# Kernel optimization log

Hardware: AMD Instinct MI355X
Metric: run time of the kernel (lower is better)

Reference implementation:

```python
import jax, jax.numpy as jnp
import numpy as np

INPUT_SIZE = 256
OUTPUT_SIZE = 128
N = 8192
SLOPE = 0.01
NEG_BIG = -9e15


def setup_inputs() -> dict:
    key = jax.random.key(0)
    k_h, k_adj, k_W, k_a = jax.random.split(key, 4)
    h = jax.random.normal(k_h, (N, INPUT_SIZE), dtype=jnp.float32)
    adj = jax.random.randint(k_adj, (N, N), 0, 2, dtype=jnp.int32)
    # xavier_uniform with gain=1.414
    gain = 1.414
    lim_W = gain * np.sqrt(6.0 / (INPUT_SIZE + OUTPUT_SIZE))
    W = jax.random.uniform(k_W, (INPUT_SIZE, OUTPUT_SIZE), dtype=jnp.float32, minval=-lim_W, maxval=lim_W)
    lim_a = gain * np.sqrt(6.0 / (2 * OUTPUT_SIZE + 1))
    a = jax.random.uniform(k_a, (2 * OUTPUT_SIZE, 1), dtype=jnp.float32, minval=-lim_a, maxval=lim_a)
    return {"h": h, "adj": adj, "W": W, "a": a}


def reference(h, adj, W, a):
    # Wh: [N, F]
    Wh = h @ W
    Fo = Wh.shape[1]
    # Original builds [N, N, 2F] concat then matmul with a; equivalent to
    # e[i, j] = leaky_relu(Wh[i] . a[:F] + Wh[j] . a[F:]) via broadcasting.
    src = Wh @ a[:Fo, 0]   # [N]
    dst = Wh @ a[Fo:, 0]   # [N]
    e = jax.nn.leaky_relu(src[:, None] + dst[None, :], negative_slope=SLOPE)  # [N, N]
    att = jnp.where(adj > 0, e, NEG_BIG)
    att = jax.nn.softmax(att, axis=1)
    return att @ Wh
```

## Files before the change

### kernel.cpp

```cpp
#include <hip/hip_runtime.h>
#include <hip/hip_bf16.h>

typedef unsigned short u16;
typedef unsigned int u32;
typedef __attribute__((ext_vector_type(8))) short short8;
typedef __attribute__((ext_vector_type(4))) float f32x4;

#define NN 8192
#define KIN 256
#define FOUT 128
#define SPLITS 8
#define KPER (NN / SPLITS)
#define BK 64
#define ITERS (KPER / BK)
#define L2E 1.4426950408889634f

__device__ __forceinline__ float exp2fast(float x) { return __builtin_amdgcn_exp2f(x); }

__device__ __forceinline__ u16 f2bf(float f) {
    u32 u = __float_as_uint(f);
    u32 r = ((u >> 16) & 1u) + 0x7fffu;
    return (u16)((u + r) >> 16);
}
__device__ __forceinline__ u32 fkey(float f) {
    u32 b = __float_as_uint(f);
    return (b & 0x80000000u) ? ~b : (b | 0x80000000u);
}
__device__ __forceinline__ float funkey(u32 k) {
    u32 b = (k & 0x80000000u) ? (k & 0x7fffffffu) : ~k;
    return __uint_as_float(b);
}

__global__ __launch_bounds__(256) void k1_wh(
    const float* __restrict__ h, const float* __restrict__ W, const float* __restrict__ a,
    u16* __restrict__ whbt,
    float* __restrict__ src, float* __restrict__ dst, u32* __restrict__ gmaxk)
{
    __shared__ float hT[64][36];
    __shared__ u16   lt[128][40];
    __shared__ float sd[32][2];
    const int t  = threadIdx.x;
    const int m0 = blockIdx.x * 32;
    const int rq = t >> 5, cq = t & 31;

    float acc[4][4];
#pragma unroll
    for (int i = 0; i < 4; i++)
#pragma unroll
        for (int j = 0; j < 4; j++) acc[i][j] = 0.f;
    if (t < 64) sd[t >> 1][t & 1] = 0.f;

    for (int kt = 0; kt < KIN; kt += 64) {
        __syncthreads();
#pragma unroll
        for (int s2 = 0; s2 < 2; s2++) {
            int f = s2 * 256 + t;
            int r = f >> 4, kc = (f & 15) * 4;
            float4 hv = *(const float4*)(h + (size_t)(m0 + r) * KIN + kt + kc);
            hT[kc + 0][r] = hv.x; hT[kc + 1][r] = hv.y;
            hT[kc + 2][r] = hv.z; hT[kc + 3][r] = hv.w;
        }
        __syncthreads();
        for (int k = 0; k < 64; k++) {
            float4 wv = *(const float4*)(W + (size_t)(kt + k) * FOUT + cq * 4);
            float h0 = hT[k][rq * 4 + 0], h1 = hT[k][rq * 4 + 1];
            float h2 = hT[k][rq * 4 + 2], h3 = hT[k][rq * 4 + 3];
            acc[0][0] += h0 * wv.x; acc[0][1] += h0 * wv.y; acc[0][2] += h0 * wv.z; acc[0][3] += h0 * wv.w;
            acc[1][0] += h1 * wv.x; acc[1][1] += h1 * wv.y; acc[1][2] += h1 * wv.z; acc[1][3] += h1 * wv.w;
            acc[2][0] += h2 * wv.x; acc[2][1] += h2 * wv.y; acc[2][2] += h2 * wv.z; acc[2][3] += h2 * wv.w;
            acc[3][0] += h3 * wv.x; acc[3][1] += h3 * wv.y; acc[3][2] += h3 * wv.z; acc[3][3] += h3 * wv.w;
        }
    }
#pragma unroll
    for (int i = 0; i < 4; i++) {
        float sp = 0.f, dp = 0.f;
#pragma unroll
        for (int j = 0; j < 4; j++) {
            sp += acc[i][j] * a[cq * 4 + j];
            dp += acc[i][j] * a[FOUT + cq * 4 + j];
            lt[cq * 4 + j][rq * 4 + i] = f2bf(acc[i][j]);
        }
        atomicAdd(&sd[rq * 4 + i][0], sp);
        atomicAdd(&sd[rq * 4 + i][1], dp);
    }
    __syncthreads();
    if (t < 32) { src[m0 + t] = sd[t][0]; dst[m0 + t] = sd[t][1]; }
    if (t < 64) {
        float v = (t < 32) ? sd[t][1] : -3.0e38f;
#pragma unroll
        for (int off = 32; off >= 1; off >>= 1) v = fmaxf(v, __shfl_down(v, off));
        if (t == 0) atomicMax(gmaxk, fkey(v));
    }
#pragma unroll
    for (int s2 = 0; s2 < 2; s2++) {
        int f = s2 * 256 + t;
        int n = f >> 2;
        int q = (f & 3) * 8;
        uint4 v = *(const uint4*)&lt[n][q];
        *(uint4*)(whbt + (size_t)n * NN + m0 + q) = v;
    }
}

__global__ __launch_bounds__(256, 2) void k2_attn(
    const int* __restrict__ adj, const float* __restrict__ src, const float* __restrict__ dst,
    const u16* __restrict__ whbt, const u32* __restrict__ gmaxk,
    float* __restrict__ accp, float* __restrict__ lp)
{
    __shared__ u16 P[128][72];
    __shared__ u16 Bs[128][72];
    __shared__ float2 sC[128];
    __shared__ float lred[128][16];
    const int t = threadIdx.x;
    const int i0 = blockIdx.x * 128;
    const int split = blockIdx.y;
    const int kb0 = split * KPER;
    const int lane = t & 63, wave = t >> 6;
    const int mw = (wave >> 1) * 64, nw = (wave & 1) * 64;
    const int l15 = lane & 15, quad = lane >> 4;
    const int g = t >> 4, c4 = (t & 15) * 4;

    if (t < 128) {
        float s = src[i0 + t] * L2E;
        float gm = funkey(*gmaxk) * L2E;
        float x = s + gm;
        sC[t] = make_float2(s, fmaxf(x, 0.01f * x));
    }
    float psum[8];
#pragma unroll
    for (int s2 = 0; s2 < 8; s2++) psum[s2] = 0.f;
    f32x4 acc[4][4];
#pragma unroll
    for (int mt = 0; mt < 4; mt++)
#pragma unroll
        for (int nt = 0; nt < 4; nt++) acc[mt][nt] = {0.f, 0.f, 0.f, 0.f};

    int4 av[8]; float4 dv; uint4 bv[4];
    {
        float4 d = *(const float4*)(dst + kb0 + c4);
        dv = make_float4(d.x * L2E, d.y * L2E, d.z * L2E, d.w * L2E);
    }
#pragma unroll
    for (int s2 = 0; s2 < 8; s2++)
        av[s2] = *(const int4*)(adj + (size_t)(i0 + 16 * s2 + g) * NN + kb0 + c4);
#pragma unroll
    for (int p = 0; p < 4; p++) {
        int f = p * 256 + t;
        int n = f >> 3, seg = (f & 7) * 8;
        bv[p] = *(const uint4*)(whbt + (size_t)n * NN + kb0 + seg);
    }

    for (int it = 0; it < ITERS; ++it) {
        const int kb = kb0 + it * BK;
        __syncthreads();
        float4 d4 = dv;
#pragma unroll
        for (int s2 = 0; s2 < 8; s2++) {
            int r = 16 * s2 + g;
            float2 sc = sC[r];
            int4 a4 = av[s2];
            float x0 = sc.x + d4.x; x0 = fmaxf(x0, 0.01f * x0);
            float x1 = sc.x + d4.y; x1 = fmaxf(x1, 0.01f * x1);
            float x2 = sc.x + d4.z; x2 = fmaxf(x2, 0.01f * x2);
            float x3 = sc.x + d4.w; x3 = fmaxf(x3, 0.01f * x3);
            float p0 = (a4.x > 0) ? exp2fast(x0 - sc.y) : 0.f;
            float p1 = (a4.y > 0) ? exp2fast(x1 - sc.y) : 0.f;
            float p2 = (a4.z > 0) ? exp2fast(x2 - sc.y) : 0.f;
            float p3 = (a4.w > 0) ? exp2fast(x3 - sc.y) : 0.f;
            psum[s2] += (p0 + p1) + (p2 + p3);
            u32 lo = (u32)f2bf(p0) | ((u32)f2bf(p1) << 16);
            u32 hi = (u32)f2bf(p2) | ((u32)f2bf(p3) << 16);
            *(uint2*)&P[r][c4] = make_uint2(lo, hi);
        }
#pragma unroll
        for (int p = 0; p < 4; p++) {
            int f = p * 256 + t;
            int n = f >> 3, seg = (f & 7) * 8;
            *(uint4*)&Bs[n][seg] = bv[p];
        }
        __syncthreads();
        if (it + 1 < ITERS) {
            int kbn = kb + BK;
            float4 d = *(const float4*)(dst + kbn + c4);
            dv = make_float4(d.x * L2E, d.y * L2E, d.z * L2E, d.w * L2E);
#pragma unroll
            for (int s2 = 0; s2 < 8; s2++)
                av[s2] = *(const int4*)(adj + (size_t)(i0 + 16 * s2 + g) * NN + kbn + c4);
#pragma unroll
            for (int p = 0; p < 4; p++) {
                int f = p * 256 + t;
                int n = f >> 3, seg = (f & 7) * 8;
                bv[p] = *(const uint4*)(whbt + (size_t)n * NN + kbn + seg);
            }
        }
#pragma unroll
        for (int ks = 0; ks < 2; ks++) {
            int kk = ks * 32 + quad * 8;
            short8 af[4], bfr[4];
#pragma unroll
            for (int mt = 0; mt < 4; mt++)
                af[mt] = *(const short8*)&P[mw + mt * 16 + l15][kk];
#pragma unroll
            for (int nt = 0; nt < 4; nt++)
                bfr[nt] = *(const short8*)&Bs[nw + nt * 16 + l15][kk];
#pragma unroll
            for (int mt = 0; mt < 4; mt++)
#pragma unroll
                for (int nt = 0; nt < 4; nt++)
                    acc[mt][nt] = __builtin_amdgcn_mfma_f32_16x16x32_bf16(
                        af[mt], bfr[nt], acc[mt][nt], 0, 0, 0);
        }
    }
    __syncthreads();
#pragma unroll
    for (int s2 = 0; s2 < 8; s2++) lred[16 * s2 + g][t & 15] = psum[s2];
    __syncthreads();
    if (t < 128) {
        float s = 0.f;
#pragma unroll
        for (int j = 0; j < 16; j++) s += lred[t][j];
        lp[split * NN + i0 + t] = s;
    }
    float* ab = accp + (size_t)split * (NN * FOUT);
#pragma unroll
    for (int mt = 0; mt < 4; mt++)
#pragma unroll
        for (int nt = 0; nt < 4; nt++) {
            int row = i0 + mw + mt * 16 + quad * 4;
            int col = nw + nt * 16 + l15;
#pragma unroll
            for (int reg = 0; reg < 4; reg++)
                ab[(size_t)(row + reg) * FOUT + col] = acc[mt][nt][reg];
        }
}

__global__ __launch_bounds__(256) void k3_comb(
    const float* __restrict__ accp, const float* __restrict__ lp, float* __restrict__ out)
{
    int idx = blockIdx.x * 256 + threadIdx.x;
    int i = idx >> 5;
    float4 s = make_float4(0.f, 0.f, 0.f, 0.f);
    float l = 0.f;
#pragma unroll
    for (int sp = 0; sp < SPLITS; sp++) {
        float4 v = *(const float4*)(accp + (size_t)sp * (NN * FOUT) + (size_t)idx * 4);
        s.x += v.x; s.y += v.y; s.z += v.z; s.w += v.w;
        l += lp[sp * NN + i];
    }
    float inv = 1.0f / l;
    *(float4*)(out + (size_t)idx * 4) = make_float4(s.x * inv, s.y * inv, s.z * inv, s.w * inv);
}

extern "C" void kernel_launch(void* const* d_in, const int* in_sizes, int n_in,
                              void* d_out, int out_size, void* d_ws, size_t ws_size,
                              hipStream_t stream) {
    const float* h   = (const float*)d_in[0];
    const int*   adj = (const int*)d_in[1];
    const float* W   = (const float*)d_in[2];
    const float* a   = (const float*)d_in[3];
    float* out = (float*)d_out;

    char* ws = (char*)d_ws;
    u16*   whbt  = (u16*)ws;
    float* src   = (float*)(ws + (2u << 20));
    float* dst   = src + NN;
    u32*   gmaxk = (u32*)(dst + NN);
    float* accp  = (float*)(ws + (3u << 20));
    float* lp    = (float*)(ws + (35u << 20));

    (void)hipMemsetAsync(gmaxk, 0, sizeof(u32), stream);
    k1_wh<<<dim3(NN / 32), dim3(256), 0, stream>>>(h, W, a, whbt, src, dst, gmaxk);
    k2_attn<<<dim3(NN / 128, SPLITS), dim3(256), 0, stream>>>(adj, src, dst, whbt, gmaxk, accp, lp);
    k3_comb<<<dim3((NN * FOUT / 4) / 256), dim3(256), 0, stream>>>(accp, lp, out);
}
```

Baseline: 482.4 us.

## Shrink attention tile to 64 rows, raise occupancy, stagger k-iterations across blocks

Halves the k2 row tile from 128 to 64 and raises the launch bound from 2 to 4 blocks per SIMD, so each wave now computes a 64x32 output slab. Adjacent blocks start their K loop at staggered offsets to spread accesses across memory channels. The leaky-relu is folded algebraically into a max of two precomputed affine terms, masking is done by clamping the exponent, and bf16 conversion uses a packed intrinsic. Partial results are stored in MFMA-native tile layout and row sums are reduced with shuffles, which adds a small row-sum kernel and a scattered-write combine step. The smaller tile doubles the Wh B-tile traffic per output row.

```diff
diff --git a/kernel.cpp b/kernel.cpp
--- a/kernel.cpp
+++ b/kernel.cpp
@@ -22,6 +22,11 @@
     u32 r = ((u >> 16) & 1u) + 0x7fffu;
     return (u16)((u + r) >> 16);
 }
+__device__ __forceinline__ u32 pk_bf16(float a, float b) {
+    union { __hip_bfloat162 h2; u32 u; } cv;
+    cv.h2 = __float22bfloat162_rn(make_float2(a, b));
+    return cv.u;
+}
 __device__ __forceinline__ u32 fkey(float f) {
     u32 b = __float_as_uint(f);
     return (b & 0x80000000u) ? ~b : (b | 0x80000000u);
@@ -101,75 +106,76 @@
     }
 }
 
-__global__ __launch_bounds__(256, 2) void k2_attn(
+__global__ __launch_bounds__(256, 4) void k2_attn(
     const int* __restrict__ adj, const float* __restrict__ src, const float* __restrict__ dst,
     const u16* __restrict__ whbt, const u32* __restrict__ gmaxk,
     float* __restrict__ accp, float* __restrict__ lp)
 {
-    __shared__ u16 P[128][72];
+    __shared__ u16 P[64][72];
     __shared__ u16 Bs[128][72];
-    __shared__ float2 sC[128];
-    __shared__ float lred[128][16];
+    __shared__ float2 sY[64];
     const int t = threadIdx.x;
-    const int i0 = blockIdx.x * 128;
+    const int bx = blockIdx.x;
+    const int i0 = bx * 64;
     const int split = blockIdx.y;
     const int kb0 = split * KPER;
     const int lane = t & 63, wave = t >> 6;
-    const int mw = (wave >> 1) * 64, nw = (wave & 1) * 64;
+    const int nw = wave * 32;
     const int l15 = lane & 15, quad = lane >> 4;
-    const int g = t >> 4, c4 = (t & 15) * 4;
-
-    if (t < 128) {
+    const int g = t >> 4;
+    const int c4 = (t & 15) * 4;
+
+    if (t < 64) {
         float s = src[i0 + t] * L2E;
         float gm = funkey(*gmaxk) * L2E;
         float x = s + gm;
-        sC[t] = make_float2(s, fmaxf(x, 0.01f * x));
-    }
-    float psum[8];
-#pragma unroll
-    for (int s2 = 0; s2 < 8; s2++) psum[s2] = 0.f;
-    f32x4 acc[4][4];
+        float C = fmaxf(x, 0.01f * x);
+        sY[t] = make_float2(s - C, 0.01f * s - C);
+    }
+    float psum[4] = {0.f, 0.f, 0.f, 0.f};
+    f32x4 acc[4][2];
 #pragma unroll
     for (int mt = 0; mt < 4; mt++)
 #pragma unroll
-        for (int nt = 0; nt < 4; nt++) acc[mt][nt] = {0.f, 0.f, 0.f, 0.f};
-
-    int4 av[8]; float4 dv; uint4 bv[4];
+        for (int nt = 0; nt < 2; nt++) acc[mt][nt] = {0.f, 0.f, 0.f, 0.f};
+
+    int itc = bx & (ITERS - 1);
+    int4 av[4]; float4 d1, d2; uint4 bv[4];
     {
-        float4 d = *(const float4*)(dst + kb0 + c4);
-        dv = make_float4(d.x * L2E, d.y * L2E, d.z * L2E, d.w * L2E);
-    }
-#pragma unroll
-    for (int s2 = 0; s2 < 8; s2++)
-        av[s2] = *(const int4*)(adj + (size_t)(i0 + 16 * s2 + g) * NN + kb0 + c4);
-#pragma unroll
-    for (int p = 0; p < 4; p++) {
-        int f = p * 256 + t;
-        int n = f >> 3, seg = (f & 7) * 8;
-        bv[p] = *(const uint4*)(whbt + (size_t)n * NN + kb0 + seg);
+        int kb = kb0 + itc * BK;
+        float4 d = *(const float4*)(dst + kb + c4);
+        d1 = make_float4(d.x * L2E, d.y * L2E, d.z * L2E, d.w * L2E);
+        d2 = make_float4(0.01f * d1.x, 0.01f * d1.y, 0.01f * d1.z, 0.01f * d1.w);
+#pragma unroll
+        for (int s2 = 0; s2 < 4; s2++)
+            av[s2] = *(const int4*)(adj + (size_t)(i0 + 16 * s2 + g) * NN + kb + c4);
+#pragma unroll
+        for (int p = 0; p < 4; p++) {
+            int f = p * 256 + t;
+            int n = f >> 3, seg = (f & 7) * 8;
+            bv[p] = *(const uint4*)(whbt + (size_t)n * NN + kb + seg);
+        }
     }
 
     for (int it = 0; it < ITERS; ++it) {
-        const int kb = kb0 + it * BK;
-        __syncthreads();
-        float4 d4 = dv;
-#pragma unroll
-        for (int s2 = 0; s2 < 8; s2++) {
+        __syncthreads();
+#pragma unroll
+        for (int s2 = 0; s2 < 4; s2++) {
             int r = 16 * s2 + g;
-            float2 sc = sC[r];
+            float2 y = sY[r];
             int4 a4 = av[s2];
-            float x0 = sc.x + d4.x; x0 = fmaxf(x0, 0.01f * x0);
-            float x1 = sc.x + d4.y; x1 = fmaxf(x1, 0.01f * x1);
-            float x2 = sc.x + d4.z; x2 = fmaxf(x2, 0.01f * x2);
-            float x3 = sc.x + d4.w; x3 = fmaxf(x3, 0.01f * x3);
-            float p0 = (a4.x > 0) ? exp2fast(x0 - sc.y) : 0.f;
-            float p1 = (a4.y > 0) ? exp2fast(x1 - sc.y) : 0.f;
-            float p2 = (a4.z > 0) ? exp2fast(x2 - sc.y) : 0.f;
-            float p3 = (a4.w > 0) ? exp2fast(x3 - sc.y) : 0.f;
+            float x0 = fmaxf(y.x + d1.x, y.y + d2.x);
+            float x1 = fmaxf(y.x + d1.y, y.y + d2.y);
+            float x2 = fmaxf(y.x + d1.z, y.y + d2.z);
+            float x3 = fmaxf(y.x + d1.w, y.y + d2.w);
+            x0 = (a4.x > 0) ? x0 : -1.0e9f;
+            x1 = (a4.y > 0) ? x1 : -1.0e9f;
+            x2 = (a4.z > 0) ? x2 : -1.0e9f;
+            x3 = (a4.w > 0) ? x3 : -1.0e9f;
+            float p0 = exp2fast(x0), p1 = exp2fast(x1);
+            float p2 = exp2fast(x2), p3 = exp2fast(x3);
             psum[s2] += (p0 + p1) + (p2 + p3);
-            u32 lo = (u32)f2bf(p0) | ((u32)f2bf(p1) << 16);
-            u32 hi = (u32)f2bf(p2) | ((u32)f2bf(p3) << 16);
-            *(uint2*)&P[r][c4] = make_uint2(lo, hi);
+            *(uint2*)&P[r][c4] = make_uint2(pk_bf16(p0, p1), pk_bf16(p2, p3));
         }
 #pragma unroll
         for (int p = 0; p < 4; p++) {
@@ -179,75 +185,88 @@
         }
         __syncthreads();
         if (it + 1 < ITERS) {
-            int kbn = kb + BK;
-            float4 d = *(const float4*)(dst + kbn + c4);
-            dv = make_float4(d.x * L2E, d.y * L2E, d.z * L2E, d.w * L2E);
-#pragma unroll
-            for (int s2 = 0; s2 < 8; s2++)
-                av[s2] = *(const int4*)(adj + (size_t)(i0 + 16 * s2 + g) * NN + kbn + c4);
+            int itn = (itc + 1) & (ITERS - 1);
+            int kb = kb0 + itn * BK;
+            float4 d = *(const float4*)(dst + kb + c4);
+            d1 = make_float4(d.x * L2E, d.y * L2E, d.z * L2E, d.w * L2E);
+            d2 = make_float4(0.01f * d1.x, 0.01f * d1.y, 0.01f * d1.z, 0.01f * d1.w);
+#pragma unroll
+            for (int s2 = 0; s2 < 4; s2++)
+                av[s2] = *(const int4*)(adj + (size_t)(i0 + 16 * s2 + g) * NN + kb + c4);
 #pragma unroll
             for (int p = 0; p < 4; p++) {
                 int f = p * 256 + t;
                 int n = f >> 3, seg = (f & 7) * 8;
-                bv[p] = *(const uint4*)(whbt + (size_t)n * NN + kbn + seg);
+                bv[p] = *(const uint4*)(whbt + (size_t)n * NN + kb + seg);
             }
+            itc = itn;
         }
 #pragma unroll
         for (int ks = 0; ks < 2; ks++) {
             int kk = ks * 32 + quad * 8;
-            short8 af[4], bfr[4];
+            short8 af[4], bfr[2];
 #pragma unroll
             for (int mt = 0; mt < 4; mt++)
-                af[mt] = *(const short8*)&P[mw + mt * 16 + l15][kk];
-#pragma unroll
-            for (int nt = 0; nt < 4; nt++)
+                af[mt] = *(const short8*)&P[mt * 16 + l15][kk];
+#pragma unroll
+            for (int nt = 0; nt < 2; nt++)
                 bfr[nt] = *(const short8*)&Bs[nw + nt * 16 + l15][kk];
 #pragma unroll
             for (int mt = 0; mt < 4; mt++)
 #pragma unroll
-                for (int nt = 0; nt < 4; nt++)
+                for (int nt = 0; nt < 2; nt++)
                     acc[mt][nt] = __builtin_amdgcn_mfma_f32_16x16x32_bf16(
                         af[mt], bfr[nt], acc[mt][nt], 0, 0, 0);
         }
     }
-    __syncthreads();
-#pragma unroll
-    for (int s2 = 0; s2 < 8; s2++) lred[16 * s2 + g][t & 15] = psum[s2];
-    __syncthreads();
-    if (t < 128) {
-        float s = 0.f;
-#pragma unroll
-        for (int j = 0; j < 16; j++) s += lred[t][j];
-        lp[split * NN + i0 + t] = s;
+#pragma unroll
+    for (int s2 = 0; s2 < 4; s2++) {
+        float v = psum[s2];
+        v += __shfl_down(v, 8, 16);
+        v += __shfl_down(v, 4, 16);
+        v += __shfl_down(v, 2, 16);
+        v += __shfl_down(v, 1, 16);
+        if ((t & 15) == 0) lp[split * NN + i0 + 16 * s2 + g] = v;
     }
     float* ab = accp + (size_t)split * (NN * FOUT);
 #pragma unroll
     for (int mt = 0; mt < 4; mt++)
 #pragma unroll
-        for (int nt = 0; nt < 4; nt++) {
-            int row = i0 + mw + mt * 16 + quad * 4;
-            int col = nw + nt * 16 + l15;
-#pragma unroll
-            for (int reg = 0; reg < 4; reg++)
-                ab[(size_t)(row + reg) * FOUT + col] = acc[mt][nt][reg];
-        }
+        for (int nt = 0; nt < 2; nt++) {
+            int tm = bx * 4 + mt;
+            int tn = wave * 2 + nt;
+            *(f32x4*)&ab[(size_t)(tm * 8 + tn) * 256 + lane * 4] = acc[mt][nt];
+        }
+}
+
+__global__ __launch_bounds__(256) void k2b_rsum(const float* __restrict__ lp,
+                                               float* __restrict__ rinv)
+{
+    int i = blockIdx.x * 256 + threadIdx.x;
+    float s = 0.f;
+#pragma unroll
+    for (int sp = 0; sp < SPLITS; sp++) s += lp[sp * NN + i];
+    rinv[i] = 1.0f / s;
 }
 
 __global__ __launch_bounds__(256) void k3_comb(
-    const float* __restrict__ accp, const float* __restrict__ lp, float* __restrict__ out)
+    const float* __restrict__ accp, const float* __restrict__ rinv, float* __restrict__ out)
 {
     int idx = blockIdx.x * 256 + threadIdx.x;
-    int i = idx >> 5;
+    int tile = idx >> 6, l = idx & 63;
     float4 s = make_float4(0.f, 0.f, 0.f, 0.f);
-    float l = 0.f;
 #pragma unroll
     for (int sp = 0; sp < SPLITS; sp++) {
         float4 v = *(const float4*)(accp + (size_t)sp * (NN * FOUT) + (size_t)idx * 4);
         s.x += v.x; s.y += v.y; s.z += v.z; s.w += v.w;
-        l += lp[sp * NN + i];
-    }
-    float inv = 1.0f / l;
-    *(float4*)(out + (size_t)idx * 4) = make_float4(s.x * inv, s.y * inv, s.z * inv, s.w * inv);
+    }
+    int row0 = (tile >> 3) * 16 + (l >> 4) * 4;
+    int col  = (tile & 7) * 16 + (l & 15);
+    float4 ri = *(const float4*)(rinv + row0);
+    out[(size_t)(row0 + 0) * FOUT + col] = s.x * ri.x;
+    out[(size_t)(row0 + 1) * FOUT + col] = s.y * ri.y;
+    out[(size_t)(row0 + 2) * FOUT + col] = s.z * ri.z;
+    out[(size_t)(row0 + 3) * FOUT + col] = s.w * ri.w;
 }
 
 extern "C" void kernel_launch(void* const* d_in, const int* in_sizes, int n_in,
@@ -266,9 +285,11 @@
     u32*   gmaxk = (u32*)(dst + NN);
     float* accp  = (float*)(ws + (3u << 20));
     float* lp    = (float*)(ws + (35u << 20));
+    float* rinv  = (float*)(ws + (36u << 20));
 
     (void)hipMemsetAsync(gmaxk, 0, sizeof(u32), stream);
     k1_wh<<<dim3(NN / 32), dim3(256), 0, stream>>>(h, W, a, whbt, src, dst, gmaxk);
-    k2_attn<<<dim3(NN / 128, SPLITS), dim3(256), 0, stream>>>(adj, src, dst, whbt, gmaxk, accp, lp);
-    k3_comb<<<dim3((NN * FOUT / 4) / 256), dim3(256), 0, stream>>>(accp, lp, out);
-}
+    k2_attn<<<dim3(NN / 64, SPLITS), dim3(256), 0, stream>>>(adj, src, dst, whbt, gmaxk, accp, lp);
+    k2b_rsum<<<dim3(NN / 256), dim3(256), 0, stream>>>(lp, rinv);
+    k3_comb<<<dim3((NN * FOUT / 4) / 256), dim3(256), 0, stream>>>(accp, rinv, out);
+}
```

Result: faster. 470.8 us (-2.4%).
